# Performance work log

Measured on AMD Instinct MI355X. Metric: run time of the kernel, lower is better.

Reference implementation:

```python
import jax, jax.numpy as jnp
import numpy as np

NHEAD = 8
HB, WB = 16, 16  # block_size


def _mha(q, k, v, w_in, b_in, w_out, b_out, nhead):
    # q,k,v: [L, B, C] seq-first, like torch.nn.MultiheadAttention (eval mode, no dropout)
    Lq, B, C = q.shape
    d = C // nhead
    wq, wk, wv = jnp.split(w_in, 3, axis=0)
    bq, bk, bv = jnp.split(b_in, 3)
    qh = (q @ wq.T + bq).reshape(Lq, B, nhead, d).transpose(1, 2, 0, 3)        # [B,H,Lq,d]
    kh = (k @ wk.T + bk).reshape(k.shape[0], B, nhead, d).transpose(1, 2, 0, 3)
    vh = (v @ wv.T + bv).reshape(v.shape[0], B, nhead, d).transpose(1, 2, 0, 3)
    scale = 1.0 / jnp.sqrt(jnp.asarray(d, dtype=qh.dtype))
    scores = jnp.einsum('bhqd,bhkd->bhqk', qh * scale, kh)
    attn = jax.nn.softmax(scores, axis=-1)
    out = jnp.einsum('bhqk,bhkd->bhqd', attn, vh)                               # [B,H,Lq,d]
    out = out.transpose(2, 0, 1, 3).reshape(Lq, B, C)
    return out @ w_out.T + b_out


def setup_inputs() -> dict:
    key = jax.random.key(0)
    ks = jax.random.split(key, 12)
    n, c, t, h, w = 2, 256, 2, 64, 64
    q = jax.random.normal(ks[0], (n, c, t, h, w), dtype=jnp.float32)
    k = jax.random.normal(ks[1], (n, c, t, h, w), dtype=jnp.float32)
    v = jax.random.normal(ks[2], (n, c, t, h, w), dtype=jnp.float32)
    pos = jax.random.normal(ks[3], (n, c, t, h, w), dtype=jnp.float32)
    s = 0.02
    wl_in = jax.random.normal(ks[4], (3 * c, c), dtype=jnp.float32) * s
    bl_in = jnp.zeros((3 * c,), dtype=jnp.float32)
    wl_out = jax.random.normal(ks[5], (c, c), dtype=jnp.float32) * s
    bl_out = jnp.zeros((c,), dtype=jnp.float32)
    ws_in = jax.random.normal(ks[6], (3 * c, c), dtype=jnp.float32) * s
    bs_in = jnp.zeros((3 * c,), dtype=jnp.float32)
    ws_out = jax.random.normal(ks[7], (c, c), dtype=jnp.float32) * s
    bs_out = jnp.zeros((c,), dtype=jnp.float32)
    return {"q": q, "k": k, "v": v, "pos": pos,
            "wl_in": wl_in, "bl_in": bl_in, "wl_out": wl_out, "bl_out": bl_out,
            "ws_in": ws_in, "bs_in": bs_in, "ws_out": ws_out, "bs_out": bs_out}


def reference(q, k, v, pos, wl_in, bl_in, wl_out, bl_out, ws_in, bs_in, ws_out, bs_out):
    n, c, t_q, h, w = q.shape
    t_k = k.shape[2]
    bn_h, bn_w = h // HB, w // WB

    def to_long(x, t):
        # [n,c,t,h,w] -> [t*bn_h*bn_w, n*HB*WB, c]
        x = x.reshape(n, c, t, bn_h, HB, bn_w, WB).transpose(2, 3, 5, 0, 4, 6, 1)
        return x.reshape(t * bn_h * bn_w, n * HB * WB, c)

    ql = to_long(q, t_q)
    kl = to_long(k, t_k)
    vl = to_long(v, t_k)
    pl = to_long(pos, t_q)

    v1 = _mha(ql + pl, kl + pl, vl, wl_in, bl_in, wl_out, bl_out, NHEAD)

    def long_to_short(x):
        # [t*bn_h*bn_w, n*HB*WB, c] -> [t*HB*WB, n*bn_h*bn_w, c]
        x = x.reshape(t_q, bn_h, bn_w, n, HB, WB, c).transpose(0, 4, 5, 3, 1, 2, 6)
        return x.reshape(t_q * HB * WB, n * bn_h * bn_w, c)

    v2 = long_to_short(v1)
    ps = long_to_short(pl)

    out = _mha(v2 + ps, v2 + ps, v2, ws_in, bs_in, ws_out, bs_out, NHEAD)
    out = out.reshape(t_q, HB, WB, n, bn_h, bn_w, c).transpose(3, 6, 0, 4, 1, 5, 2)
    return out.reshape(n, c, t_q, h, w)
```

## Files before the change

kernel.cpp:

```cpp
#include <hip/hip_runtime.h>
#include <math.h>


#define SCALE_D32 0.17677669529663687f
#define EXP2_SCALE 0.25508680987930193f
#define GLOBAL_AS __attribute__((address_space(1)))
#define LDS_AS __attribute__((address_space(3)))

typedef short short8 __attribute__((ext_vector_type(8)));
typedef short short4v __attribute__((ext_vector_type(4)));
typedef short short2v __attribute__((ext_vector_type(2)));
typedef float floatx4 __attribute__((ext_vector_type(4)));

__device__ __forceinline__ short f2bf(float f) {
  union { float f; unsigned u; } x;
  x.f = f;
  unsigned r = x.u + 0x7fffu + ((x.u >> 16) & 1u);
  return (short)(r >> 16);
}
__device__ __forceinline__ float bf2f(short s) {
  union { unsigned u; float f; } x;
  x.u = ((unsigned)(unsigned short)s) << 16;
  return x.f;
}

__device__ __forceinline__ int o1s_phys(int q, int ch) {
  return q * 256 + (ch & ~63) + ((((ch >> 3) & 7) ^ (q & 7)) << 3) + (ch & 7);
}

__global__ __launch_bounds__(256) void pack_kernel(
    const float* __restrict__ q, const float* __restrict__ k,
    const float* __restrict__ v, const float* __restrict__ pos,
    short* __restrict__ Xp, short* __restrict__ Xq,
    short* __restrict__ Xk, short* __restrict__ Xv,
    const float* __restrict__ wl_in, const float* __restrict__ wl_out,
    const float* __restrict__ ws_in, const float* __restrict__ ws_out,
    short* __restrict__ wbf) {
  __shared__ float tP[64][65];
  __shared__ float tX[64][65];
  int b = blockIdx.x;
  int cb = b & 3;
  int h  = (b >> 2) & 63;
  int nt = b >> 8;
  int n = nt >> 1, t = nt & 1;
  int c0 = cb * 64;
  int bh = h >> 4, ii = h & 15;
  long inbase = (long)n * 2097152 + (long)t * 4096 + (long)h * 64;
  int tx = threadIdx.x & 63;
  int ty = threadIdx.x >> 6;

  for (int cc = ty; cc < 64; cc += 4) {
    long a = inbase + (long)(c0 + cc) * 8192 + tx;
    tP[cc][tx] = pos[a];
    tX[cc][tx] = q[a];
  }
  __syncthreads();
  for (int ww = ty; ww < 64; ww += 4) {
    int bw = ww >> 4, j = ww & 15;
    int m1 = (((t * 4 + bh) * 4 + bw) * 512) + n * 256 + ii * 16 + j;
    long o = (long)m1 * 256 + c0 + tx;
    float pv = tP[tx][ww];
    Xp[o] = f2bf(pv);
    Xq[o] = f2bf(tX[tx][ww] + pv);
  }
  __syncthreads();
  for (int cc = ty; cc < 64; cc += 4) {
    long a = inbase + (long)(c0 + cc) * 8192 + tx;
    tX[cc][tx] = k[a];
  }
  __syncthreads();
  for (int ww = ty; ww < 64; ww += 4) {
    int bw = ww >> 4, j = ww & 15;
    int m1 = (((t * 4 + bh) * 4 + bw) * 512) + n * 256 + ii * 16 + j;
    long o = (long)m1 * 256 + c0 + tx;
    Xk[o] = f2bf(tX[tx][ww] + tP[tx][ww]);
  }
  __syncthreads();
  for (int cc = ty; cc < 64; cc += 4) {
    long a = inbase + (long)(c0 + cc) * 8192 + tx;
    tX[cc][tx] = v[a];
  }
  __syncthreads();
  for (int ww = ty; ww < 64; ww += 4) {
    int bw = ww >> 4, j = ww & 15;
    int m1 = (((t * 4 + bh) * 4 + bw) * 512) + n * 256 + ii * 16 + j;
    long o = (long)m1 * 256 + c0 + tx;
    Xv[o] = f2bf(tX[tx][ww]);
  }
  int idx = (blockIdx.x * 256 + threadIdx.x) * 2;
  const float* wp;
  if (idx < 196608) wp = wl_in + idx;
  else if (idx < 262144) wp = wl_out + (idx - 196608);
  else if (idx < 458752) wp = ws_in + (idx - 262144);
  else wp = ws_out + (idx - 458752);
  float2 wv = *(const float2*)wp;
  wbf[idx] = f2bf(wv.x);
  wbf[idx + 1] = f2bf(wv.y);
}

template <bool OUT32>
__global__ __launch_bounds__(256) void gemm_tri(
    const short* __restrict__ A0, const short* __restrict__ A1,
    const short* __restrict__ A2, const short* __restrict__ W0,
    const float* __restrict__ bias0, void* __restrict__ C0,
    void* __restrict__ C1, void* __restrict__ C2) {
  __shared__ short As[128 * 64];
  __shared__ short Ws[64 * 64];
  int z = blockIdx.z;
  const short* A = (z == 0) ? A0 : ((z == 1) ? A1 : A2);
  const short* Wb = W0 + z * 65536;
  const float* bias = bias0 + z * 256;
  void* Csel = (z == 0) ? C0 : ((z == 1) ? C1 : C2);
  int m0 = blockIdx.x * 128;
  int n0 = blockIdx.y * 64;
  int tid = threadIdx.x;
  int lane = tid & 63, wave = tid >> 6;
  int wm = wave >> 1, wn = wave & 1;
  int l15 = lane & 15, quad = lane >> 4;
  int x7 = l15 & 7;
  int rsub = lane >> 3;
  int csub = lane & 7;

  floatx4 acc[4][2];
#pragma unroll
  for (int mt = 0; mt < 4; ++mt)
#pragma unroll
    for (int nt = 0; nt < 2; ++nt) acc[mt][nt] = (floatx4)(0.f);

  for (int kb = 0; kb < 4; ++kb) {
    int k0 = kb * 64;
    if (kb) __syncthreads();
#pragma unroll
    for (int j = 0; j < 4; ++j) {
      int r0 = (wave * 4 + j) * 8;
      int row = r0 + rsub;
      int c = csub ^ (row & 7);
      const short* gp = A + (long)(m0 + row) * 256 + k0 + c * 8;
      short* lp = &As[r0 * 64 + lane * 8];
      __builtin_amdgcn_global_load_lds((const GLOBAL_AS void*)gp,
                                       (LDS_AS void*)lp, 16, 0, 0);
    }
#pragma unroll
    for (int j = 0; j < 2; ++j) {
      int r0 = (wave * 2 + j) * 8;
      int row = r0 + rsub;
      int c = csub ^ (row & 7);
      const short* gp = Wb + (long)(n0 + row) * 256 + k0 + c * 8;
      short* lp = &Ws[r0 * 64 + lane * 8];
      __builtin_amdgcn_global_load_lds((const GLOBAL_AS void*)gp,
                                       (LDS_AS void*)lp, 16, 0, 0);
    }
    __syncthreads();
#pragma unroll
    for (int ks = 0; ks < 2; ++ks) {
      int pc = (ks * 4 + quad) ^ x7;
      short8 af[4], bfr[2];
#pragma unroll
      for (int mt = 0; mt < 4; ++mt) {
        int row = wm * 64 + mt * 16 + l15;
        af[mt] = *(const short8*)&As[row * 64 + pc * 8];
      }
#pragma unroll
      for (int nt = 0; nt < 2; ++nt) {
        int row = wn * 32 + nt * 16 + l15;
        bfr[nt] = *(const short8*)&Ws[row * 64 + pc * 8];
      }
#pragma unroll
      for (int mt = 0; mt < 4; ++mt)
#pragma unroll
        for (int nt = 0; nt < 2; ++nt)
          acc[mt][nt] = __builtin_amdgcn_mfma_f32_16x16x32_bf16(
              af[mt], bfr[nt], acc[mt][nt], 0, 0, 0);
    }
  }
  float bia0 = bias[n0 + wn * 32 + l15];
  float bia1 = bias[n0 + wn * 32 + 16 + l15];
#pragma unroll
  for (int mt = 0; mt < 4; ++mt) {
#pragma unroll
    for (int r = 0; r < 4; ++r) {
      int row = m0 + wm * 64 + mt * 16 + quad * 4 + r;
      long base = (long)row * 256 + n0 + wn * 32 + l15;
      if (OUT32) {
        float* C = (float*)Csel;
        C[base] = acc[mt][0][r] + bia0;
        C[base + 16] = acc[mt][1][r] + bia1;
      } else {
        short* C = (short*)Csel;
        C[base] = f2bf(acc[mt][0][r] + bia0);
        C[base + 16] = f2bf(acc[mt][1][r] + bia1);
      }
    }
  }
}

__global__ __launch_bounds__(256) void attn1_fused(
    const short* __restrict__ Q1, const short* __restrict__ K1,
    const short* __restrict__ V1, const short* __restrict__ Xp,
    const short* __restrict__ Wo, const float* __restrict__ bias,
    short* __restrict__ X2, short* __restrict__ V2in) {
  __shared__ union {
    struct {
      short Vs[32][264];
      short Vt[4][32][40];
      short Pw[4][32][40];
    } a;
    struct {
      short O1s[32 * 256];
      short Ws[256 * 64];
    } g;
  } u;
  int b1 = blockIdx.x;
  int tid = threadIdx.x;
  int wave = tid >> 6, lane = tid & 63;
  int l15 = lane & 15, quad = lane >> 4;
  int x7 = l15 & 7;
  int rsub = lane >> 3;
  int csub = lane & 7;

#pragma unroll
  for (int p = 0; p < 4; ++p) {
    int idx = p * 256 + tid;
    int row = idx >> 5;
    int c8 = idx & 31;
    *(short8*)&u.a.Vs[row][c8 * 8] =
        *(const short8*)(V1 + ((long)row * 512 + b1) * 256 + c8 * 8);
  }
  __syncthreads();

  int key = lane & 31;
  int dh = (lane >> 5) * 16;
  int pc2 = 2 * (key & 15) + (key >> 4);

  floatx4 oacc[2][4];
  float lsum[2][2][4];

#pragma unroll
  for (int h2 = 0; h2 < 2; ++h2) {
    int hh = wave * 2 + h2;
    long fbase = ((long)l15 * 512 + b1) * 256 + hh * 32 + quad * 8;
    short8 qf0 = *(const short8*)(Q1 + fbase);
    short8 qf1 = *(const short8*)(Q1 + fbase + 16 * 512 * 256);
    short8 kf0 = *(const short8*)(K1 + fbase);
    short8 kf1 = *(const short8*)(K1 + fbase + 16 * 512 * 256);
    short8 v0 = *(const short8*)&u.a.Vs[key][hh * 32 + dh];
    short8 v1 = *(const short8*)&u.a.Vs[key][hh * 32 + dh + 8];
#pragma unroll
    for (int j = 0; j < 8; ++j) {
      u.a.Vt[wave][dh + j][pc2] = v0[j];
      u.a.Vt[wave][dh + 8 + j][pc2] = v1[j];
    }
    floatx4 s00 = __builtin_amdgcn_mfma_f32_16x16x32_bf16(qf0, kf0, (floatx4)(0.f), 0, 0, 0);
    floatx4 s01 = __builtin_amdgcn_mfma_f32_16x16x32_bf16(qf0, kf1, (floatx4)(0.f), 0, 0, 0);
    floatx4 s10 = __builtin_amdgcn_mfma_f32_16x16x32_bf16(qf1, kf0, (floatx4)(0.f), 0, 0, 0);
    floatx4 s11 = __builtin_amdgcn_mfma_f32_16x16x32_bf16(qf1, kf1, (floatx4)(0.f), 0, 0, 0);
    float li0[4], li1[4];
#pragma unroll
    for (int r = 0; r < 4; ++r) {
      float p00 = __builtin_amdgcn_exp2f(s00[r] * EXP2_SCALE);
      float p01 = __builtin_amdgcn_exp2f(s01[r] * EXP2_SCALE);
      float p10 = __builtin_amdgcn_exp2f(s10[r] * EXP2_SCALE);
      float p11 = __builtin_amdgcn_exp2f(s11[r] * EXP2_SCALE);
      li0[r] = p00 + p01;
      li1[r] = p10 + p11;
      short2v pa, pb;
      pa.x = f2bf(p00); pa.y = f2bf(p01);
      pb.x = f2bf(p10); pb.y = f2bf(p11);
      *(short2v*)&u.a.Pw[wave][quad * 4 + r][2 * l15] = pa;
      *(short2v*)&u.a.Pw[wave][16 + quad * 4 + r][2 * l15] = pb;
    }
#pragma unroll
    for (int r = 0; r < 4; ++r) {
      li0[r] += __shfl_xor(li0[r], 1, 64);
      li0[r] += __shfl_xor(li0[r], 2, 64);
      li0[r] += __shfl_xor(li0[r], 4, 64);
      li0[r] += __shfl_xor(li0[r], 8, 64);
      li1[r] += __shfl_xor(li1[r], 1, 64);
      li1[r] += __shfl_xor(li1[r], 2, 64);
      li1[r] += __shfl_xor(li1[r], 4, 64);
      li1[r] += __shfl_xor(li1[r], 8, 64);
      lsum[h2][0][r] = li0[r];
      lsum[h2][1][r] = li1[r];
    }
    short8 pf0 = *(const short8*)&u.a.Pw[wave][l15][quad * 8];
    short8 pf1 = *(const short8*)&u.a.Pw[wave][16 + l15][quad * 8];
    short8 vt0 = *(const short8*)&u.a.Vt[wave][l15][quad * 8];
    short8 vt1 = *(const short8*)&u.a.Vt[wave][16 + l15][quad * 8];
    oacc[h2][0] = __builtin_amdgcn_mfma_f32_16x16x32_bf16(pf0, vt0, (floatx4)(0.f), 0, 0, 0);
    oacc[h2][1] = __builtin_amdgcn_mfma_f32_16x16x32_bf16(pf0, vt1, (floatx4)(0.f), 0, 0, 0);
    oacc[h2][2] = __builtin_amdgcn_mfma_f32_16x16x32_bf16(pf1, vt0, (floatx4)(0.f), 0, 0, 0);
    oacc[h2][3] = __builtin_amdgcn_mfma_f32_16x16x32_bf16(pf1, vt1, (floatx4)(0.f), 0, 0, 0);
  }

  __syncthreads();

#pragma unroll
  for (int h2 = 0; h2 < 2; ++h2) {
    int hh = wave * 2 + h2;
    int cA = hh * 32 + l15;
    int cB = cA + 16;
#pragma unroll
    for (int r = 0; r < 4; ++r) {
      float inv0 = 1.f / lsum[h2][0][r];
      float inv1 = 1.f / lsum[h2][1][r];
      int qa = quad * 4 + r, qb = 16 + quad * 4 + r;
      u.g.O1s[o1s_phys(qa, cA)] = f2bf(oacc[h2][0][r] * inv0);
      u.g.O1s[o1s_phys(qa, cB)] = f2bf(oacc[h2][1][r] * inv0);
      u.g.O1s[o1s_phys(qb, cA)] = f2bf(oacc[h2][2][r] * inv1);
      u.g.O1s[o1s_phys(qb, cB)] = f2bf(oacc[h2][3][r] * inv1);
    }
  }

  floatx4 acc[2][4];
#pragma unroll
  for (int mt = 0; mt < 2; ++mt)
#pragma unroll
    for (int nt = 0; nt < 4; ++nt) acc[mt][nt] = (floatx4)(0.f);

  for (int kb = 0; kb < 4; ++kb) {
    __syncthreads();
#pragma unroll
    for (int j = 0; j < 8; ++j) {
      int r0 = (wave * 8 + j) * 8;
      int row = r0 + rsub;
      int c = csub ^ (row & 7);
      const short* gp = Wo + (long)row * 256 + kb * 64 + c * 8;
      short* lp = &u.g.Ws[r0 * 64 + lane * 8];
      __builtin_amdgcn_global_load_lds((const GLOBAL_AS void*)gp,
                                       (LDS_AS void*)lp, 16, 0, 0);
    }
    __syncthreads();
#pragma unroll
    for (int ks = 0; ks < 2; ++ks) {
      int pc = (ks * 4 + quad) ^ x7;
      short8 af[2], bfr[4];
#pragma unroll
      for (int mt = 0; mt < 2; ++mt)
        af[mt] = *(const short8*)&u.g.O1s[(mt * 16 + l15) * 256 + kb * 64 + pc * 8];
#pragma unroll
      for (int nt = 0; nt < 4; ++nt)
        bfr[nt] = *(const short8*)&u.g.Ws[(wave * 64 + nt * 16 + l15) * 64 + pc * 8];
#pragma unroll
      for (int mt = 0; mt < 2; ++mt)
#pragma unroll
        for (int nt = 0; nt < 4; ++nt)
          acc[mt][nt] = __builtin_amdgcn_mfma_f32_16x16x32_bf16(
              af[mt], bfr[nt], acc[mt][nt], 0, 0, 0);
    }
  }

  int nn = b1 >> 8, ii = (b1 >> 4) & 15, jj = b1 & 15;
  float bv[4];
#pragma unroll
  for (int nt = 0; nt < 4; ++nt) bv[nt] = bias[wave * 64 + nt * 16 + l15];
#pragma unroll
  for (int mt = 0; mt < 2; ++mt) {
#pragma unroll
    for (int r = 0; r < 4; ++r) {
      int qrow = mt * 16 + quad * 4 + r;
      int t = qrow >> 4, bh = (qrow >> 2) & 3, bw = qrow & 3;
      int m2 = (t * 256 + ii * 16 + jj) * 32 + nn * 16 + bh * 4 + bw;
      long xbase = (long)m2 * 256;
      long pbase = ((long)qrow * 512 + b1) * 256;
#pragma unroll
      for (int nt = 0; nt < 4; ++nt) {
        int col = wave * 64 + nt * 16 + l15;
        float val = acc[mt][nt][r] + bv[nt];
        X2[xbase + col] = f2bf(val + bf2f(Xp[pbase + col]));
        V2in[xbase + col] = f2bf(val);
      }
    }
  }
}

__global__ __launch_bounds__(256) void attn2_mfma(
    const short* __restrict__ Q2, const short* __restrict__ K2,
    const short* __restrict__ V2, short* __restrict__ O2) {
  __shared__ short Ks[64][40];
  __shared__ short Vt[32][72];
  __shared__ short Pw[4][16][72];
  int bid = blockIdx.x;
  int rest = bid & 255;
  int qblk = bid >> 8;
  int hh = 2 * (rest & 3) + (rest >> 7);
  int b2 = (rest >> 2) & 31;
  int tid = threadIdx.x;
  int wave = tid >> 6, lane = tid & 63;
  int l15 = lane & 15, quad = lane >> 4;

  short8 qf;
  {
    long tok = (long)(qblk * 64 + wave * 16 + l15) * 32 + b2;
    qf = *(const short8*)(Q2 + tok * 256 + hh * 32 + quad * 8);
  }
  floatx4 Oa = (floatx4)(0.f), Ob = (floatx4)(0.f);
  float li[4] = {0.f, 0.f, 0.f, 0.f};

  int skey = tid >> 2;
  int sd0 = (tid & 3) * 8;
  int vkey = lane;
  int vd0 = wave * 8;
  int vcol = (vkey & 15) * 4 + (vkey >> 4);

  for (int kb = 0; kb < 8; ++kb) {
    if (kb) __syncthreads();
    {
      long tok = (long)(kb * 64 + skey) * 32 + b2;
      *(short8*)&Ks[skey][sd0] = *(const short8*)(K2 + tok * 256 + hh * 32 + sd0);
    }
    {
      long tok = (long)(kb * 64 + vkey) * 32 + b2;
      short8 v = *(const short8*)(V2 + tok * 256 + hh * 32 + vd0);
#pragma unroll
      for (int j = 0; j < 8; ++j) Vt[vd0 + j][vcol] = v[j];
    }
    __syncthreads();
    floatx4 st[4];
#pragma unroll
    for (int kt = 0; kt < 4; ++kt) {
      short8 kf = *(const short8*)&Ks[kt * 16 + l15][quad * 8];
      st[kt] = __builtin_amdgcn_mfma_f32_16x16x32_bf16(qf, kf, (floatx4)(0.f), 0, 0, 0);
    }
#pragma unroll
    for (int r = 0; r < 4; ++r) {
      float p0 = __builtin_amdgcn_exp2f(st[0][r] * EXP2_SCALE);
      float p1 = __builtin_amdgcn_exp2f(st[1][r] * EXP2_SCALE);
      float p2 = __builtin_amdgcn_exp2f(st[2][r] * EXP2_SCALE);
      float p3 = __builtin_amdgcn_exp2f(st[3][r] * EXP2_SCALE);
      li[r] += (p0 + p1) + (p2 + p3);
      short4v pp;
      pp.x = f2bf(p0); pp.y = f2bf(p1); pp.z = f2bf(p2); pp.w = f2bf(p3);
      *(short4v*)&Pw[wave][quad * 4 + r][l15 * 4] = pp;
    }
#pragma unroll
    for (int kk = 0; kk < 2; ++kk) {
      short8 pf = *(const short8*)&Pw[wave][l15][kk * 32 + quad * 8];
      short8 v0 = *(const short8*)&Vt[l15][kk * 32 + quad * 8];
      short8 v1 = *(const short8*)&Vt[16 + l15][kk * 32 + quad * 8];
      Oa = __builtin_amdgcn_mfma_f32_16x16x32_bf16(pf, v0, Oa, 0, 0, 0);
      Ob = __builtin_amdgcn_mfma_f32_16x16x32_bf16(pf, v1, Ob, 0, 0, 0);
    }
  }
#pragma unroll
  for (int r = 0; r < 4; ++r) {
    float s = li[r];
    s += __shfl_xor(s, 1, 64);
    s += __shfl_xor(s, 2, 64);
    s += __shfl_xor(s, 4, 64);
    s += __shfl_xor(s, 8, 64);
    float inv = 1.f / s;
    long tok = (long)(qblk * 64 + wave * 16 + quad * 4 + r) * 32 + b2;
    long a = tok * 256 + hh * 32 + l15;
    O2[a] = f2bf(Oa[r] * inv);
    O2[a + 16] = f2bf(Ob[r] * inv);
  }
}

__global__ __launch_bounds__(256) void unpack_kernel(
    const float* __restrict__ Y, float* __restrict__ out) {
  __shared__ float tl[64][65];
  int b = blockIdx.x;
  int cb = b & 3;
  int h = (b >> 2) & 63;
  int nt = b >> 8;
  int n = nt >> 1, t = nt & 1;
  int c0 = cb * 64;
  int bh = h >> 4, ii = h & 15;
  int tx = threadIdx.x & 63;
  int ty = threadIdx.x >> 6;
  for (int ww = ty; ww < 64; ww += 4) {
    int bw = ww >> 4, j = ww & 15;
    int l2 = t * 256 + ii * 16 + j;
    int b2 = n * 16 + bh * 4 + bw;
    int m2 = l2 * 32 + b2;
    tl[tx][ww] = Y[(long)m2 * 256 + c0 + tx];
  }
  __syncthreads();
  long ob = (long)n * 2097152 + (long)t * 4096 + (long)h * 64 + tx;
  for (int cc = ty; cc < 64; cc += 4) {
    out[ob + (long)(c0 + cc) * 8192] = tl[cc][tx];
  }
}

extern "C" void kernel_launch(void* const* d_in, const int* in_sizes, int n_in,
                              void* d_out, int out_size, void* d_ws, size_t ws_size,
                              hipStream_t stream) {
  const float* q      = (const float*)d_in[0];
  const float* k      = (const float*)d_in[1];
  const float* v      = (const float*)d_in[2];
  const float* pos    = (const float*)d_in[3];
  const float* wl_in  = (const float*)d_in[4];
  const float* bl_in  = (const float*)d_in[5];
  const float* wl_out = (const float*)d_in[6];
  const float* bl_out = (const float*)d_in[7];
  const float* ws_in  = (const float*)d_in[8];
  const float* bs_in  = (const float*)d_in[9];
  const float* ws_out = (const float*)d_in[10];
  const float* bs_out = (const float*)d_in[11];
  float* out = (float*)d_out;
  char* wsb = (char*)d_ws;
  const size_t SLB = 16777216;
  short* s0 = (short*)(wsb);
  short* wbf = (short*)(wsb + SLB / 2);
  short* s1 = (short*)(wsb + SLB);
  short* s2 = (short*)(wsb + 2 * SLB);
  short* s3 = (short*)(wsb + 3 * SLB);
  short* s4 = (short*)(wsb + 4 * SLB);
  short* s5 = (short*)(wsb + 5 * SLB);
  short* s6 = (short*)(wsb + 6 * SLB);

  pack_kernel<<<1024, 256, 0, stream>>>(q, k, v, pos, s0, s1, s2, s3,
                                        wl_in, wl_out, ws_in, ws_out, wbf);

  dim3 g3(128, 4, 3);
  dim3 g1(128, 4, 1);
  gemm_tri<false><<<g3, 256, 0, stream>>>(s1, s2, s3, wbf, bl_in, s4, s5, s6);

  attn1_fused<<<512, 256, 0, stream>>>(s4, s5, s6, s0, wbf + 196608, bl_out,
                                       s3, s2);

  gemm_tri<false><<<g3, 256, 0, stream>>>(s3, s3, s2, wbf + 262144, bs_in,
                                          s5, s6, s1);

  attn2_mfma<<<2048, 256, 0, stream>>>(s5, s6, s1, s3);
  gemm_tri<true><<<g1, 256, 0, stream>>>(s3, s3, s3, wbf + 458752, bs_out,
                                         s2, s2, s2);

  unpack_kernel<<<1024, 256, 0, stream>>>((const float*)s2, out);
}
```

Measured before the change: 209.5 us.

## Fuse second-stage QKV input projection into attention-1 kernel

The short-attention Q/K/V projection GEMM is folded into the attention-1 kernel. Each block keeps its 32-row output-projection result (with and without the positional term) in LDS and multiplies it by the three input-projection weight matrices, writing Q2/K2/V2 directly. This drops one kernel launch and the global round trip of the intermediate X2/V2in tensors. The cost is extra LDS (16 KB more), which may reduce occupancy. Each block also re-streams 3×256×256 weights with no overlap between weight loads and MFMA work, and the GEMM tile is small.

```diff
diff --git a/kernel.cpp b/kernel.cpp
--- a/kernel.cpp
+++ b/kernel.cpp
@@ -26,6 +26,20 @@
 
 __device__ __forceinline__ int o1s_phys(int q, int ch) {
   return q * 256 + (ch & ~63) + ((((ch >> 3) & 7) ^ (q & 7)) << 3) + (ch & 7);
+}
+
+__device__ __forceinline__ void stage_w(short* Wsl, const short* Wg, int kb,
+                                        int wave, int lane, int rsub, int csub) {
+#pragma unroll
+  for (int j = 0; j < 8; ++j) {
+    int r0 = (wave * 8 + j) * 8;
+    int row = r0 + rsub;
+    int c = csub ^ (row & 7);
+    const short* gp = Wg + (long)row * 256 + kb * 64 + c * 8;
+    short* lp = &Wsl[r0 * 64 + lane * 8];
+    __builtin_amdgcn_global_load_lds((const GLOBAL_AS void*)gp,
+                                     (LDS_AS void*)lp, 16, 0, 0);
+  }
 }
 
 __global__ __launch_bounds__(256) void pack_kernel(
@@ -194,11 +208,12 @@
   }
 }
 
-__global__ __launch_bounds__(256) void attn1_fused(
+__global__ __launch_bounds__(256) void attn1_mega(
     const short* __restrict__ Q1, const short* __restrict__ K1,
     const short* __restrict__ V1, const short* __restrict__ Xp,
-    const short* __restrict__ Wo, const float* __restrict__ bias,
-    short* __restrict__ X2, short* __restrict__ V2in) {
+    const short* __restrict__ Wo, const float* __restrict__ bias_o,
+    const short* __restrict__ Wsin, const float* __restrict__ bias_sin,
+    short* __restrict__ Q2, short* __restrict__ K2, short* __restrict__ V2) {
   __shared__ union {
     struct {
       short Vs[32][264];
@@ -207,6 +222,7 @@
     } a;
     struct {
       short O1s[32 * 256];
+      short Vins[32 * 256];
       short Ws[256 * 64];
     } g;
   } u;
@@ -311,24 +327,15 @@
     }
   }
 
-  floatx4 acc[2][4];
+  floatx4 acc1[2][4];
 #pragma unroll
   for (int mt = 0; mt < 2; ++mt)
 #pragma unroll
-    for (int nt = 0; nt < 4; ++nt) acc[mt][nt] = (floatx4)(0.f);
+    for (int nt = 0; nt < 4; ++nt) acc1[mt][nt] = (floatx4)(0.f);
 
   for (int kb = 0; kb < 4; ++kb) {
     __syncthreads();
-#pragma unroll
-    for (int j = 0; j < 8; ++j) {
-      int r0 = (wave * 8 + j) * 8;
-      int row = r0 + rsub;
-      int c = csub ^ (row & 7);
-      const short* gp = Wo + (long)row * 256 + kb * 64 + c * 8;
-      short* lp = &u.g.Ws[r0 * 64 + lane * 8];
-      __builtin_amdgcn_global_load_lds((const GLOBAL_AS void*)gp,
-                                       (LDS_AS void*)lp, 16, 0, 0);
-    }
+    stage_w(u.g.Ws, Wo, kb, wave, lane, rsub, csub);
     __syncthreads();
 #pragma unroll
     for (int ks = 0; ks < 2; ++ks) {
@@ -344,30 +351,87 @@
       for (int mt = 0; mt < 2; ++mt)
 #pragma unroll
         for (int nt = 0; nt < 4; ++nt)
-          acc[mt][nt] = __builtin_amdgcn_mfma_f32_16x16x32_bf16(
-              af[mt], bfr[nt], acc[mt][nt], 0, 0, 0);
+          acc1[mt][nt] = __builtin_amdgcn_mfma_f32_16x16x32_bf16(
+              af[mt], bfr[nt], acc1[mt][nt], 0, 0, 0);
+    }
+  }
+
+  __syncthreads();
+  {
+    float bvo[4];
+#pragma unroll
+    for (int nt = 0; nt < 4; ++nt) bvo[nt] = bias_o[wave * 64 + nt * 16 + l15];
+#pragma unroll
+    for (int mt = 0; mt < 2; ++mt) {
+#pragma unroll
+      for (int r = 0; r < 4; ++r) {
+        int qrow = mt * 16 + quad * 4 + r;
+        long pbase = ((long)qrow * 512 + b1) * 256;
+#pragma unroll
+        for (int nt = 0; nt < 4; ++nt) {
+          int col = wave * 64 + nt * 16 + l15;
+          float val = acc1[mt][nt][r] + bvo[nt];
+          int ph = o1s_phys(qrow, col);
+          u.g.Vins[ph] = f2bf(val);
+          u.g.O1s[ph] = f2bf(val + bf2f(Xp[pbase + col]));
+        }
+      }
     }
   }
 
   int nn = b1 >> 8, ii = (b1 >> 4) & 15, jj = b1 & 15;
-  float bv[4];
-#pragma unroll
-  for (int nt = 0; nt < 4; ++nt) bv[nt] = bias[wave * 64 + nt * 16 + l15];
-#pragma unroll
-  for (int mt = 0; mt < 2; ++mt) {
-#pragma unroll
-    for (int r = 0; r < 4; ++r) {
-      int qrow = mt * 16 + quad * 4 + r;
-      int t = qrow >> 4, bh = (qrow >> 2) & 3, bw = qrow & 3;
-      int m2 = (t * 256 + ii * 16 + jj) * 32 + nn * 16 + bh * 4 + bw;
-      long xbase = (long)m2 * 256;
-      long pbase = ((long)qrow * 512 + b1) * 256;
-#pragma unroll
-      for (int nt = 0; nt < 4; ++nt) {
-        int col = wave * 64 + nt * 16 + l15;
-        float val = acc[mt][nt][r] + bv[nt];
-        X2[xbase + col] = f2bf(val + bf2f(Xp[pbase + col]));
-        V2in[xbase + col] = f2bf(val);
+#pragma unroll
+  for (int z = 0; z < 3; ++z) {
+    const short* Wz = Wsin + z * 65536;
+    const short* Ab = (z < 2) ? (const short*)u.g.O1s : (const short*)u.g.Vins;
+    short* outz = (z == 0) ? Q2 : ((z == 1) ? K2 : V2);
+    float bz[4];
+#pragma unroll
+    for (int nt = 0; nt < 4; ++nt)
+      bz[nt] = bias_sin[z * 256 + wave * 64 + nt * 16 + l15];
+
+    floatx4 acc[2][4];
+#pragma unroll
+    for (int mt = 0; mt < 2; ++mt)
+#pragma unroll
+      for (int nt = 0; nt < 4; ++nt) acc[mt][nt] = (floatx4)(0.f);
+
+    for (int kb = 0; kb < 4; ++kb) {
+      __syncthreads();
+      stage_w(u.g.Ws, Wz, kb, wave, lane, rsub, csub);
+      __syncthreads();
+#pragma unroll
+      for (int ks = 0; ks < 2; ++ks) {
+        int pc = (ks * 4 + quad) ^ x7;
+        short8 af[2], bfr[4];
+#pragma unroll
+        for (int mt = 0; mt < 2; ++mt)
+          af[mt] = *(const short8*)&Ab[(mt * 16 + l15) * 256 + kb * 64 + pc * 8];
+#pragma unroll
+        for (int nt = 0; nt < 4; ++nt)
+          bfr[nt] = *(const short8*)&u.g.Ws[(wave * 64 + nt * 16 + l15) * 64 + pc * 8];
+#pragma unroll
+        for (int mt = 0; mt < 2; ++mt)
+#pragma unroll
+          for (int nt = 0; nt < 4; ++nt)
+            acc[mt][nt] = __builtin_amdgcn_mfma_f32_16x16x32_bf16(
+                af[mt], bfr[nt], acc[mt][nt], 0, 0, 0);
+      }
+    }
+
+#pragma unroll
+    for (int mt = 0; mt < 2; ++mt) {
+#pragma unroll
+      for (int r = 0; r < 4; ++r) {
+        int qrow = mt * 16 + quad * 4 + r;
+        int t = qrow >> 4, bh = (qrow >> 2) & 3, bw = qrow & 3;
+        int m2 = (t * 256 + ii * 16 + jj) * 32 + nn * 16 + bh * 4 + bw;
+        long xbase = (long)m2 * 256;
+#pragma unroll
+        for (int nt = 0; nt < 4; ++nt) {
+          int col = wave * 64 + nt * 16 + l15;
+          outz[xbase + col] = f2bf(acc[mt][nt][r] + bz[nt]);
+        }
       }
     }
   }
@@ -516,14 +580,11 @@
   dim3 g1(128, 4, 1);
   gemm_tri<false><<<g3, 256, 0, stream>>>(s1, s2, s3, wbf, bl_in, s4, s5, s6);
 
-  attn1_fused<<<512, 256, 0, stream>>>(s4, s5, s6, s0, wbf + 196608, bl_out,
-                                       s3, s2);
-
-  gemm_tri<false><<<g3, 256, 0, stream>>>(s3, s3, s2, wbf + 262144, bs_in,
-                                          s5, s6, s1);
-
-  attn2_mfma<<<2048, 256, 0, stream>>>(s5, s6, s1, s3);
-  gemm_tri<true><<<g1, 256, 0, stream>>>(s3, s3, s3, wbf + 458752, bs_out,
+  attn1_mega<<<512, 256, 0, stream>>>(s4, s5, s6, s0, wbf + 196608, bl_out,
+                                      wbf + 262144, bs_in, s1, s2, s3);
+
+  attn2_mfma<<<2048, 256, 0, stream>>>(s1, s2, s3, s4);
+  gemm_tri<true><<<g1, 256, 0, stream>>>(s4, s4, s4, wbf + 458752, bs_out,
                                          s2, s2, s2);
 
   unpack_kernel<<<1024, 256, 0, stream>>>((const float*)s2, out);
```

Result: faster. 203.1 us (-3.0%).
